# Kernel tuning notes

Measured on AMD Instinct MI355X. Metric: run time of the kernel, lower is better.

## Reference

```python
import jax, jax.numpy as jnp
from jax import lax
import numpy as np

B, N = 16, 4096
NPOINT, RADIUS, NSAMPLE = 1024, 0.2, 32
IN_CH = 64
MLP = [64, 64, 128]
EPS = 1e-5  # torch BatchNorm2d default


def setup_inputs() -> dict:
    key = jax.random.key(0)
    ks = jax.random.split(key, 2 + 2 * len(MLP))
    inp = {
        "xyz": jax.random.uniform(ks[0], (B, 3, N), jnp.float32),
        "points": jax.random.normal(ks[1], (B, IN_CH, N), jnp.float32),
    }
    last = IN_CH + 3
    for i, out in enumerate(MLP):
        inp[f"W{i}"] = jax.random.normal(ks[2 + 2 * i], (last, out), jnp.float32) / np.float32(np.sqrt(last))
        inp[f"b{i}"] = jnp.zeros((out,), jnp.float32)
        inp[f"g{i}"] = jnp.ones((out,), jnp.float32)
        inp[f"be{i}"] = jnp.zeros((out,), jnp.float32)
        last = out
    return inp


def _fps(x):
    """Farthest point sampling. x: [B,N,3] -> [B,NPOINT] int32 (start idx 0)."""
    Bv, Nn, _ = x.shape

    def step(carry, _):
        dist, far = carry
        c = jnp.take_along_axis(x, far[:, None, None], axis=1)  # [B,1,3]
        d = jnp.sum((x - c) ** 2, axis=-1)                      # [B,N]
        dist = jnp.minimum(dist, d)
        return (dist, jnp.argmax(dist, axis=-1).astype(jnp.int32)), far

    init = (jnp.full((Bv, Nn), 1e10, x.dtype), jnp.zeros((Bv,), jnp.int32))
    _, cent = lax.scan(step, init, None, length=NPOINT)
    return cent.T  # [B, NPOINT]


def _ball_query(x, new_xyz):
    """x: [B,N,3], new_xyz: [B,S,3] -> idx [B,S,NSAMPLE] int32."""
    Nn = x.shape[1]
    sqr = jnp.sum((new_xyz[:, :, None, :] - x[:, None, :, :]) ** 2, axis=-1)  # [B,S,N]
    idx = jnp.where(sqr > RADIUS ** 2, Nn, jnp.arange(Nn, dtype=jnp.int32))
    idx = jnp.sort(idx, axis=-1)[:, :, :NSAMPLE]  # first NSAMPLE in-radius indices
    first = idx[:, :, :1]
    return jnp.where(idx == Nn, first, idx)


def _gather(pts, idx):
    """pts: [B,N,C], idx: [B,S,K] -> [B,S,K,C]."""
    Bv, S, K = idx.shape
    flat = idx.reshape(Bv, S * K)
    return jnp.take_along_axis(pts, flat[:, :, None], axis=1).reshape(Bv, S, K, pts.shape[-1])


def _forward(xyz, points, params):
    x = xyz.transpose(0, 2, 1)      # [B,N,3]
    p = points.transpose(0, 2, 1)   # [B,N,D]
    fps_idx = _fps(x)
    new_xyz = jnp.take_along_axis(x, fps_idx[:, :, None], axis=1)  # [B,S,3]
    idx = _ball_query(x, new_xyz)
    g_xyz = _gather(x, idx) - new_xyz[:, :, None, :]               # [B,S,K,3]
    feats = jnp.concatenate([g_xyz, _gather(p, idx)], axis=-1)     # [B,S,K,3+D]
    for (W, b, g, be) in params:
        feats = jnp.einsum('bskc,cd->bskd', feats, W) + b          # 1x1 conv
        mean = feats.mean(axis=(0, 1, 2))                          # BN train-mode batch stats
        var = feats.var(axis=(0, 1, 2))
        feats = jax.nn.relu(g * (feats - mean) * lax.rsqrt(var + EPS) + be)
    new_points = feats.max(axis=2).transpose(0, 2, 1)              # max over nsample -> [B,C',S]
    return new_xyz.transpose(0, 2, 1), new_points


def reference(xyz, points, W0, b0, g0, be0, W1, b1, g1, be1, W2, b2, g2, be2):
    params = [(W0, b0, g0, be0), (W1, b1, g1, be1), (W2, b2, g2, be2)]
    return _forward(xyz, points, params)
```

## Files before the change

kernel.cpp:

```cpp
#include <hip/hip_runtime.h>
#include <hip/hip_bf16.h>
#include <cstdint>


typedef __attribute__((ext_vector_type(8))) short bf16x8;
typedef __attribute__((ext_vector_type(4))) float f32x4;

#define LDA 104

__device__ __forceinline__ unsigned short f2bf(float f) {
  unsigned x = __float_as_uint(f);
  unsigned r = (x + 0x7FFFu + ((x >> 16) & 1u)) >> 16;
  return (unsigned short)r;
}
__device__ __forceinline__ float bf2f(unsigned short u) {
  return __uint_as_float(((unsigned)u) << 16);
}

template <int CTRL>
__device__ __forceinline__ unsigned long long dppmax(unsigned long long k) {
  int lo = (int)(unsigned)k;
  int hi = (int)(unsigned)(k >> 32);
  int plo = __builtin_amdgcn_update_dpp(lo, lo, CTRL, 0xF, 0xF, false);
  int phi = __builtin_amdgcn_update_dpp(hi, hi, CTRL, 0xF, 0xF, false);
  unsigned long long o =
      ((unsigned long long)(unsigned)phi << 32) | (unsigned)plo;
  return (o > k) ? o : k;
}

__global__ __attribute__((amdgpu_flat_work_group_size(256, 256),
                          amdgpu_waves_per_eu(1, 1)))
void fps_prep_kernel(
    const float* __restrict__ xyz, const float* __restrict__ points,
    const float* __restrict__ W0, const float* __restrict__ W1,
    const float* __restrict__ W2, unsigned short* __restrict__ pT,
    unsigned short* __restrict__ w0t, unsigned short* __restrict__ w1t,
    unsigned short* __restrict__ w2t, float* __restrict__ stats_all,
    float* __restrict__ out, float4* __restrict__ centers4)
{
  __shared__ __align__(16) char smraw[61568];
  int tid = threadIdx.x;
  if (blockIdx.x >= 16) {
    int pb = blockIdx.x - 16;
    if (pb < 1024) {
      float (*tile)[65] = (float (*)[65])smraw;
      int b = pb >> 6;
      int n0 = (pb & 63) << 6;
      const float* pbp = points + ((size_t)b << 18);
      for (int i = tid; i < 4096; i += 256) {
        int cc = i >> 6, nn = i & 63;
        tile[cc][nn] = pbp[((size_t)cc << 12) + n0 + nn];
      }
      __syncthreads();
      for (int i = tid; i < 4096; i += 256) {
        int nn = i >> 6, cc = i & 63;
        pT[(((size_t)((b << 12) + n0 + nn)) << 6) + cc] = f2bf(tile[cc][nn]);
      }
    } else {
      for (int i = tid; i < 27136; i += 256) {
        if (i < 6656) {
          int nn = i / 104, kk = i % 104;
          float v = (kk < 64) ? W0[(3 + kk) * 64 + nn]
                              : ((kk < 67) ? W0[(kk - 64) * 64 + nn] : 0.f);
          w0t[i] = f2bf(v);
        } else if (i < 13312) {
          int j = i - 6656; int nn = j / 104, kk = j % 104;
          float v = (kk < 64) ? W1[kk * 64 + nn] : 0.f;
          w1t[j] = f2bf(v);
        } else if (i < 26624) {
          int j = i - 13312; int nn = j / 104, kk = j % 104;
          float v = (kk < 64) ? W2[kk * 128 + nn] : 0.f;
          w2t[j] = f2bf(v);
        } else {
          stats_all[i - 26624] = 0.f;
        }
      }
    }
    return;
  }
  float* xs  = (float*)smraw;
  float* ys  = xs + 4096;
  float* zs  = ys + 4096;
  float* cxl = zs + 4096;
  float* cyl = cxl + 1024;
  float* czl = cyl + 1024;
  unsigned long long (*keybuf)[4] =
      (unsigned long long (*)[4])(smraw + 61440);

  int b = blockIdx.x;
  const float* xb = xyz + (size_t)b * 12288;
  float px[16], py[16], pz[16], dist[16];
#pragma unroll
  for (int j = 0; j < 16; ++j) {
    int n = tid + (j << 8);
    px[j] = xb[n]; py[j] = xb[4096 + n]; pz[j] = xb[8192 + n];
    xs[n] = px[j]; ys[n] = py[j]; zs[n] = pz[j];
    dist[j] = 1e10f;
  }
  __syncthreads();
  float cx = xs[0], cy = ys[0], cz = zs[0];
  if (tid == 0) { cxl[0] = cx; cyl[0] = cy; czl[0] = cz; }
  int w = tid >> 6;
  int lane = tid & 63;
  for (int it = 1; it < 1024; ++it) {
    float bv = -1.f; int bi = 0;
#pragma unroll
    for (int j = 0; j < 16; ++j) {
      float dx = __fsub_rn(px[j], cx);
      float dy = __fsub_rn(py[j], cy);
      float dz = __fsub_rn(pz[j], cz);
      float d  = __fadd_rn(__fadd_rn(__fmul_rn(dx, dx), __fmul_rn(dy, dy)),
                           __fmul_rn(dz, dz));
      float nd = fminf(dist[j], d);
      dist[j] = nd;
      if (nd > bv) { bv = nd; bi = tid + (j << 8); }
    }
    unsigned long long k =
        ((unsigned long long)__float_as_uint(bv) << 32) | (unsigned)(~bi);
    k = dppmax<0xB1>(k);
    k = dppmax<0x4E>(k);
    k = dppmax<0x141>(k);
    k = dppmax<0x140>(k);
    k = dppmax<0x142>(k);
    k = dppmax<0x143>(k);
    int p = it & 1;
    if (lane == 63) keybuf[p][w] = k;
    __syncthreads();
    uint4 ka2 = *(const uint4*)&keybuf[p][0];
    uint4 kb2 = *(const uint4*)&keybuf[p][2];
    unsigned long long k0 = ((unsigned long long)ka2.y << 32) | ka2.x;
    unsigned long long k1 = ((unsigned long long)ka2.w << 32) | ka2.z;
    unsigned long long k2 = ((unsigned long long)kb2.y << 32) | kb2.x;
    unsigned long long k3 = ((unsigned long long)kb2.w << 32) | kb2.z;
    unsigned long long m01 = (k1 > k0) ? k1 : k0;
    unsigned long long m23 = (k3 > k2) ? k3 : k2;
    unsigned long long km  = (m23 > m01) ? m23 : m01;
    int gi = (int)(~(unsigned)km) & 4095;
    cx = xs[gi]; cy = ys[gi]; cz = zs[gi];
    if (tid == 0) { cxl[it] = cx; cyl[it] = cy; czl[it] = cz; }
  }
  __syncthreads();
  for (int it = tid; it < 1024; it += 256) {
    float x = cxl[it], y = cyl[it], z = czl[it];
    out[b * 3072 + it]        = x;
    out[b * 3072 + 1024 + it] = y;
    out[b * 3072 + 2048 + it] = z;
    centers4[(b << 10) + it]  = make_float4(x, y, z, 0.f);
  }
}

__global__ __launch_bounds__(256) void ball_kernel(const float* __restrict__ xyz,
                                                   const float4* __restrict__ centers4,
                                                   int* __restrict__ ballidx)
{
  __shared__ float xs[4096], ys[4096], zs[4096];
  int tid = threadIdx.x;
  int b = blockIdx.x >> 4;
  int g = blockIdx.x & 15;
  const float* xb = xyz + (size_t)b * 12288;
  for (int i = tid; i < 4096; i += 256) {
    xs[i] = xb[i]; ys[i] = xb[4096 + i]; zs[i] = xb[8192 + i];
  }
  __syncthreads();
  int w = tid >> 6, lane = tid & 63;
  unsigned long long lmask = (1ull << lane) - 1ull;
  for (int j = 0; j < 16; ++j) {
    int s = (g << 6) + (j << 2) + w;
    float4 c = centers4[(b << 10) + s];
    int* ob = ballidx + (((size_t)((b << 10) + s)) << 5);
    int cnt = 0, first = 0;
    for (int m = 0; m < 64; ++m) {
      int n = (m << 6) + lane;
      float dx = __fsub_rn(xs[n], c.x);
      float dy = __fsub_rn(ys[n], c.y);
      float dz = __fsub_rn(zs[n], c.z);
      float d  = __fadd_rn(__fadd_rn(__fmul_rn(dx, dx), __fmul_rn(dy, dy)),
                           __fmul_rn(dz, dz));
      bool hit = !(d > 0.04f);
      unsigned long long mask = __ballot(hit);
      if (cnt == 0 && mask != 0ull)
        first = (m << 6) + (__ffsll((long long)mask) - 1);
      int p = cnt + (int)__popcll(mask & lmask);
      if (hit && p < 32) ob[p] = n;
      cnt += (int)__popcll(mask);
      if (cnt >= 32) break;
    }
    if (lane < 32 && lane >= cnt) ob[lane] = first;
  }
}

__global__ __launch_bounds__(256) void gemm1_kernel(
    const float* __restrict__ xyz, const unsigned short* __restrict__ pT,
    const unsigned short* __restrict__ w0t, const float* __restrict__ b0,
    const float4* __restrict__ centers4, const int* __restrict__ ballidx,
    unsigned short* __restrict__ feats1, float* __restrict__ partials)
{
  __shared__ unsigned short As[64 * LDA];
  __shared__ unsigned short Wt[64 * LDA];
  __shared__ float red[2][4][64];
  int tid = threadIdx.x;
  int rowbase = blockIdx.x << 6;
  int b = rowbase >> 15;
  {
    const uint4* wsrc = (const uint4*)w0t;
    uint4* wdst = (uint4*)Wt;
    for (int i = tid; i < 832; i += 256) wdst[i] = wsrc[i];
  }
  {
    int rl = tid >> 2, part = tid & 3;
    int r = rowbase + rl;
    int n = ballidx[r];
    const uint4* psrc = (const uint4*)(pT + (((size_t)((b << 12) + n)) << 6));
    uint4* adst = (uint4*)(As + rl * LDA);
    adst[part * 2]     = psrc[part * 2];
    adst[part * 2 + 1] = psrc[part * 2 + 1];
    adst[8 + part] = make_uint4(0, 0, 0, 0);
    if (part == 0) {
      int ci = r >> 5;
      float4 c = centers4[ci];
      unsigned short* arow = As + rl * LDA;
      arow[64] = f2bf(__fsub_rn(xyz[(size_t)b * 12288 + n],        c.x));
      arow[65] = f2bf(__fsub_rn(xyz[(size_t)b * 12288 + 4096 + n], c.y));
      arow[66] = f2bf(__fsub_rn(xyz[(size_t)b * 12288 + 8192 + n], c.z));
    }
  }
  __syncthreads();
  int lane = tid & 63, w = tid >> 6;
  int mrow = (w << 4) + (lane & 15);
  int quad = lane >> 4;
  f32x4 acc[4];
#pragma unroll
  for (int nt = 0; nt < 4; ++nt) acc[nt] = (f32x4){0.f, 0.f, 0.f, 0.f};
#pragma unroll
  for (int kt = 0; kt < 3; ++kt) {
    int ko = kt * 32 + (quad << 3);
    bf16x8 a = *(const bf16x8*)(As + mrow * LDA + ko);
#pragma unroll
    for (int nt = 0; nt < 4; ++nt) {
      bf16x8 bb = *(const bf16x8*)(Wt + ((nt << 4) + (lane & 15)) * LDA + ko);
      acc[nt] = __builtin_amdgcn_mfma_f32_16x16x32_bf16(a, bb, acc[nt], 0, 0, 0);
    }
  }
#pragma unroll
  for (int nt = 0; nt < 4; ++nt) {
    int cch = (nt << 4) + (lane & 15);
    float bias = b0[cch];
    float ssum = 0.f, sq = 0.f;
#pragma unroll
    for (int r2 = 0; r2 < 4; ++r2) {
      float y = acc[nt][r2] + bias;
      int ml = (w << 4) + (quad << 2) + r2;
      feats1[(((size_t)(rowbase + ml)) << 6) + cch] = f2bf(y);
      ssum += y; sq += y * y;
    }
    ssum += __shfl_xor(ssum, 16); ssum += __shfl_xor(ssum, 32);
    sq   += __shfl_xor(sq, 16);   sq   += __shfl_xor(sq, 32);
    if (quad == 0) { red[0][w][cch] = ssum; red[1][w][cch] = sq; }
  }
  __syncthreads();
  if (tid < 64) {
    float a0 = red[0][0][tid] + red[0][1][tid] + red[0][2][tid] + red[0][3][tid];
    float a1 = red[1][0][tid] + red[1][1][tid] + red[1][2][tid] + red[1][3][tid];
    partials[(size_t)blockIdx.x * 256 + tid]      = a0;
    partials[(size_t)blockIdx.x * 256 + 64 + tid] = a1;
  }
}

__global__ __launch_bounds__(256) void gemm2_kernel(
    const unsigned short* __restrict__ featsIn, const unsigned short* __restrict__ wt,
    const float* __restrict__ bias_g, const float* __restrict__ ss_in,
    unsigned short* __restrict__ featsOut, float* __restrict__ partials)
{
  __shared__ unsigned short As[64 * LDA];
  __shared__ unsigned short Wt[64 * LDA];
  __shared__ float red[2][4][64];
  __shared__ float ssl[128];
  int tid = threadIdx.x;
  int rowbase = blockIdx.x << 6;
  if (tid < 128) ssl[tid] = ss_in[tid];
  {
    const uint4* wsrc = (const uint4*)wt;
    uint4* wdst = (uint4*)Wt;
    for (int i = tid; i < 832; i += 256) wdst[i] = wsrc[i];
  }
  __syncthreads();
  {
    int rl = tid >> 2, part = tid & 3;
    size_t r = (size_t)rowbase + rl;
    union { uint4 v[2]; unsigned short u[16]; } t;
    const uint4* src = (const uint4*)(featsIn + (r << 6));
    t.v[0] = src[part * 2]; t.v[1] = src[part * 2 + 1];
    union { uint4 v[2]; unsigned short u[16]; } o;
#pragma unroll
    for (int e = 0; e < 16; ++e) {
      int cch = (part << 4) + e;
      float f = bf2f(t.u[e]);
      float y = fmaxf(f * ssl[cch] + ssl[64 + cch], 0.f);
      o.u[e] = f2bf(y);
    }
    uint4* adst = (uint4*)(As + rl * LDA + (part << 4));
    adst[0] = o.v[0]; adst[1] = o.v[1];
  }
  __syncthreads();
  int lane = tid & 63, w = tid >> 6;
  int mrow = (w << 4) + (lane & 15);
  int quad = lane >> 4;
  f32x4 acc[4];
#pragma unroll
  for (int nt = 0; nt < 4; ++nt) acc[nt] = (f32x4){0.f, 0.f, 0.f, 0.f};
#pragma unroll
  for (int kt = 0; kt < 2; ++kt) {
    int ko = kt * 32 + (quad << 3);
    bf16x8 a = *(const bf16x8*)(As + mrow * LDA + ko);
#pragma unroll
    for (int nt = 0; nt < 4; ++nt) {
      bf16x8 bb = *(const bf16x8*)(Wt + ((nt << 4) + (lane & 15)) * LDA + ko);
      acc[nt] = __builtin_amdgcn_mfma_f32_16x16x32_bf16(a, bb, acc[nt], 0, 0, 0);
    }
  }
#pragma unroll
  for (int nt = 0; nt < 4; ++nt) {
    int cch = (nt << 4) + (lane & 15);
    float bias = bias_g[cch];
    float ssum = 0.f, sq = 0.f;
#pragma unroll
    for (int r2 = 0; r2 < 4; ++r2) {
      float y = acc[nt][r2] + bias;
      int ml = (w << 4) + (quad << 2) + r2;
      featsOut[(((size_t)(rowbase + ml)) << 6) + cch] = f2bf(y);
      ssum += y; sq += y * y;
    }
    ssum += __shfl_xor(ssum, 16); ssum += __shfl_xor(ssum, 32);
    sq   += __shfl_xor(sq, 16);   sq   += __shfl_xor(sq, 32);
    if (quad == 0) { red[0][w][cch] = ssum; red[1][w][cch] = sq; }
  }
  __syncthreads();
  if (tid < 64) {
    float a0 = red[0][0][tid] + red[0][1][tid] + red[0][2][tid] + red[0][3][tid];
    float a1 = red[1][0][tid] + red[1][1][tid] + red[1][2][tid] + red[1][3][tid];
    partials[(size_t)blockIdx.x * 256 + tid]      = a0;
    partials[(size_t)blockIdx.x * 256 + 64 + tid] = a1;
  }
}

__global__ __launch_bounds__(256) void gemm3_stats_kernel(
    const unsigned short* __restrict__ feats2, const unsigned short* __restrict__ w2t,
    const float* __restrict__ b2, const float* __restrict__ ss2,
    float* __restrict__ partials)
{
  __shared__ unsigned short As[64 * LDA];
  __shared__ unsigned short Wt[128 * LDA];
  __shared__ float red[2][4][128];
  __shared__ float ssl[128];
  int tid = threadIdx.x;
  int rowbase = blockIdx.x << 6;
  if (tid < 128) ssl[tid] = ss2[tid];
  {
    const uint4* wsrc = (const uint4*)w2t;
    uint4* wdst = (uint4*)Wt;
    for (int i = tid; i < 1664; i += 256) wdst[i] = wsrc[i];
  }
  __syncthreads();
  {
    int rl = tid >> 2, part = tid & 3;
    size_t r = (size_t)rowbase + rl;
    union { uint4 v[2]; unsigned short u[16]; } t;
    const uint4* src = (const uint4*)(feats2 + (r << 6));
    t.v[0] = src[part * 2]; t.v[1] = src[part * 2 + 1];
    union { uint4 v[2]; unsigned short u[16]; } o;
#pragma unroll
    for (int e = 0; e < 16; ++e) {
      int cch = (part << 4) + e;
      float f = bf2f(t.u[e]);
      float y = fmaxf(f * ssl[cch] + ssl[64 + cch], 0.f);
      o.u[e] = f2bf(y);
    }
    uint4* adst = (uint4*)(As + rl * LDA + (part << 4));
    adst[0] = o.v[0]; adst[1] = o.v[1];
  }
  __syncthreads();
  int lane = tid & 63, w = tid >> 6;
  int mrow = (w << 4) + (lane & 15);
  int quad = lane >> 4;
  f32x4 acc[8];
#pragma unroll
  for (int nt = 0; nt < 8; ++nt) acc[nt] = (f32x4){0.f, 0.f, 0.f, 0.f};
#pragma unroll
  for (int kt = 0; kt < 2; ++kt) {
    int ko = kt * 32 + (quad << 3);
    bf16x8 a = *(const bf16x8*)(As + mrow * LDA + ko);
#pragma unroll
    for (int nt = 0; nt < 8; ++nt) {
      bf16x8 bb = *(const bf16x8*)(Wt + ((nt << 4) + (lane & 15)) * LDA + ko);
      acc[nt] = __builtin_amdgcn_mfma_f32_16x16x32_bf16(a, bb, acc[nt], 0, 0, 0);
    }
  }
#pragma unroll
  for (int nt = 0; nt < 8; ++nt) {
    int cch = (nt << 4) + (lane & 15);
    float bias = b2[cch];
    float ssum = 0.f, sq = 0.f;
#pragma unroll
    for (int r2 = 0; r2 < 4; ++r2) {
      float y = acc[nt][r2] + bias;
      ssum += y; sq += y * y;
    }
    ssum += __shfl_xor(ssum, 16); ssum += __shfl_xor(ssum, 32);
    sq   += __shfl_xor(sq, 16);   sq   += __shfl_xor(sq, 32);
    if (quad == 0) { red[0][w][cch] = ssum; red[1][w][cch] = sq; }
  }
  __syncthreads();
  if (tid < 128) {
    float a0 = red[0][0][tid] + red[0][1][tid] + red[0][2][tid] + red[0][3][tid];
    float a1 = red[1][0][tid] + red[1][1][tid] + red[1][2][tid] + red[1][3][tid];
    partials[(size_t)blockIdx.x * 256 + tid]       = a0;
    partials[(size_t)blockIdx.x * 256 + 128 + tid] = a1;
  }
}

__global__ __launch_bounds__(256) void final_kernel(
    const unsigned short* __restrict__ feats2, const unsigned short* __restrict__ w2t,
    const float* __restrict__ b2, const float* __restrict__ ss2,
    const float* __restrict__ ss3, float* __restrict__ out_tmp)
{
  __shared__ unsigned short As[64 * LDA];
  __shared__ unsigned short Wt[128 * LDA];
  __shared__ float ssl[128];
  __shared__ unsigned mx[2][128];
  int tid = threadIdx.x;
  int rowbase = blockIdx.x << 6;
  if (tid < 128) ssl[tid] = ss2[tid];
  ((unsigned*)mx)[tid] = 0u;
  {
    const uint4* wsrc = (const uint4*)w2t;
    uint4* wdst = (uint4*)Wt;
    for (int i = tid; i < 1664; i += 256) wdst[i] = wsrc[i];
  }
  __syncthreads();
  {
    int rl = tid >> 2, part = tid & 3;
    size_t r = (size_t)rowbase + rl;
    union { uint4 v[2]; unsigned short u[16]; } t;
    const uint4* src = (const uint4*)(feats2 + (r << 6));
    t.v[0] = src[part * 2]; t.v[1] = src[part * 2 + 1];
    union { uint4 v[2]; unsigned short u[16]; } o;
#pragma unroll
    for (int e = 0; e < 16; ++e) {
      int cch = (part << 4) + e;
      float f = bf2f(t.u[e]);
      float y = fmaxf(f * ssl[cch] + ssl[64 + cch], 0.f);
      o.u[e] = f2bf(y);
    }
    uint4* adst = (uint4*)(As + rl * LDA + (part << 4));
    adst[0] = o.v[0]; adst[1] = o.v[1];
  }
  __syncthreads();
  int lane = tid & 63, w = tid >> 6;
  int mrow = (w << 4) + (lane & 15);
  int quad = lane >> 4;
  f32x4 acc[8];
#pragma unroll
  for (int nt = 0; nt < 8; ++nt) acc[nt] = (f32x4){0.f, 0.f, 0.f, 0.f};
#pragma unroll
  for (int kt = 0; kt < 2; ++kt) {
    int ko = kt * 32 + (quad << 3);
    bf16x8 a = *(const bf16x8*)(As + mrow * LDA + ko);
#pragma unroll
    for (int nt = 0; nt < 8; ++nt) {
      bf16x8 bb = *(const bf16x8*)(Wt + ((nt << 4) + (lane & 15)) * LDA + ko);
      acc[nt] = __builtin_amdgcn_mfma_f32_16x16x32_bf16(a, bb, acc[nt], 0, 0, 0);
    }
  }
  int cloc = w >> 1;
#pragma unroll
  for (int nt = 0; nt < 8; ++nt) {
    int cch = (nt << 4) + (lane & 15);
    float bias = b2[cch];
    float sc = ss3[cch], sh = ss3[128 + cch];
    float m = 0.f;
#pragma unroll
    for (int r2 = 0; r2 < 4; ++r2) {
      float y = acc[nt][r2] + bias;
      float tv = fmaxf(y * sc + sh, 0.f);
      m = fmaxf(m, tv);
    }
    atomicMax(&mx[cloc][cch], __float_as_uint(m));
  }
  __syncthreads();
  {
    int c2 = tid >> 7, cch = tid & 127;
    float v = __uint_as_float(mx[c2][cch]);
    int cg = (rowbase >> 5) + c2;
    out_tmp[((size_t)cg << 7) + cch] = v;
  }
}

__global__ __launch_bounds__(256) void reduce_kernel(const float* __restrict__ partials,
                                                     float* __restrict__ stats, int twoC)
{
  int tid = threadIdx.x;
  if (tid < twoC) {
    int row0 = blockIdx.x << 7;
    float s = 0.f;
    for (int r = 0; r < 128; ++r) s += partials[((size_t)(row0 + r)) * 256 + tid];
    atomicAdd(&stats[tid], s);
  }
}

__global__ void finalize_kernel(const float* __restrict__ stats, const float* __restrict__ g,
                                const float* __restrict__ be, float* __restrict__ ss, int C)
{
  int c = threadIdx.x;
  if (c < C) {
    const float invM = 1.f / 524288.f;
    float mean = stats[c] * invM;
    float ex2  = stats[C + c] * invM;
    float var  = ex2 - mean * mean;
    float sc   = g[c] / sqrtf(var + 1e-5f);
    ss[c]     = sc;
    ss[C + c] = be[c] - mean * sc;
  }
}

__global__ __launch_bounds__(256) void transpose_out_kernel(const float* __restrict__ out_tmp,
                                                            float* __restrict__ out)
{
  __shared__ float t2[64][65];
  int tid = threadIdx.x;
  int b = blockIdx.x >> 5;
  int rest = blockIdx.x & 31;
  int s0 = (rest & 15) << 6;
  int c0 = (rest >> 4) << 6;
  for (int i = tid; i < 4096; i += 256) {
    int row = i >> 6, col = i & 63;
    t2[row][col] = out_tmp[((size_t)((b << 10) + s0 + row)) * 128 + c0 + col];
  }
  __syncthreads();
  for (int i = tid; i < 4096; i += 256) {
    int crow = i >> 6, scol = i & 63;
    out[49152 + ((size_t)b << 17) + (size_t)(c0 + crow) * 1024 + s0 + scol] = t2[scol][crow];
  }
}

extern "C" void kernel_launch(void* const* d_in, const int* in_sizes, int n_in,
                              void* d_out, int out_size, void* d_ws, size_t ws_size,
                              hipStream_t stream)
{
  (void)in_sizes; (void)n_in; (void)out_size; (void)ws_size;
  const float* xyz    = (const float*)d_in[0];
  const float* points = (const float*)d_in[1];
  const float* W0  = (const float*)d_in[2];
  const float* b0  = (const float*)d_in[3];
  const float* g0  = (const float*)d_in[4];
  const float* be0 = (const float*)d_in[5];
  const float* W1  = (const float*)d_in[6];
  const float* b1  = (const float*)d_in[7];
  const float* g1  = (const float*)d_in[8];
  const float* be1 = (const float*)d_in[9];
  const float* W2  = (const float*)d_in[10];
  const float* b2  = (const float*)d_in[11];
  const float* g2  = (const float*)d_in[12];
  const float* be2 = (const float*)d_in[13];
  float* out = (float*)d_out;

  char* base = (char*)d_ws;
  size_t off = 0;
  auto alloc = [&](size_t bytes) -> void* {
    void* p = base + off;
    off += (bytes + 255) & ~(size_t)255;
    return p;
  };
  unsigned short* pT     = (unsigned short*)alloc((size_t)16 * 4096 * 64 * 2);
  unsigned short* w0t    = (unsigned short*)alloc(64 * LDA * 2);
  unsigned short* w1t    = (unsigned short*)alloc(64 * LDA * 2);
  unsigned short* w2t    = (unsigned short*)alloc(128 * LDA * 2);
  float* stats_all       = (float*)alloc(512 * 4);
  float* ss_all          = (float*)alloc(512 * 4);
  float4* centers4       = (float4*)alloc((size_t)16 * 1024 * 16);
  int* ballidx           = (int*)alloc((size_t)16 * 1024 * 32 * 4);
  unsigned short* feats1 = (unsigned short*)alloc((size_t)524288 * 64 * 2);
  unsigned short* feats2 = (unsigned short*)alloc((size_t)524288 * 64 * 2);
  float* partials        = (float*)alloc((size_t)8192 * 256 * 4);
  float* out_tmp         = (float*)alloc((size_t)16 * 1024 * 128 * 4);

  float* stats1 = stats_all;       float* stats2 = stats_all + 128; float* stats3 = stats_all + 256;
  float* ss1 = ss_all;             float* ss2 = ss_all + 128;       float* ss3 = ss_all + 256;

  fps_prep_kernel<<<1041, 256, 0, stream>>>(xyz, points, W0, W1, W2, pT, w0t, w1t,
                                            w2t, stats_all, out, centers4);
  ball_kernel<<<256, 256, 0, stream>>>(xyz, centers4, ballidx);
  gemm1_kernel<<<8192, 256, 0, stream>>>(xyz, pT, w0t, b0, centers4, ballidx, feats1, partials);
  reduce_kernel<<<64, 256, 0, stream>>>(partials, stats1, 128);
  finalize_kernel<<<1, 64, 0, stream>>>(stats1, g0, be0, ss1, 64);
  gemm2_kernel<<<8192, 256, 0, stream>>>(feats1, w1t, b1, ss1, feats2, partials);
  reduce_kernel<<<64, 256, 0, stream>>>(partials, stats2, 128);
  finalize_kernel<<<1, 64, 0, stream>>>(stats2, g1, be1, ss2, 64);
  gemm3_stats_kernel<<<8192, 256, 0, stream>>>(feats2, w2t, b2, ss2, partials);
  reduce_kernel<<<64, 256, 0, stream>>>(partials, stats3, 256);
  finalize_kernel<<<1, 128, 0, stream>>>(stats3, g2, be2, ss3, 128);
  final_kernel<<<8192, 256, 0, stream>>>(feats2, w2t, b2, ss2, ss3, out_tmp);
  transpose_out_kernel<<<512, 256, 0, stream>>>(out_tmp, out);
}
```

Baseline: 967.8 us.

## Drop GEMM3 recompute by tracking per-group max/min pre-BN outputs

The gemm3 stats kernel now also records, for each sample group and channel, the max and min of the pre-BN layer-3 output. Because BN followed by ReLU is monotone per channel, the final max can be taken from the max or the min depending on the sign of the scale. This removes the second full GEMM pass over feats2 (final_kernel), and the transpose kernel applies the affine step and ReLU instead. It adds extra writes of two 8 MB buffers, placed in the now-unused feats1 region.

After: 942.3 us. 1.03x faster.

```diff
diff --git a/kernel.cpp b/kernel.cpp
--- a/kernel.cpp
+++ b/kernel.cpp
@@ -346,11 +346,14 @@
 __global__ __launch_bounds__(256) void gemm3_stats_kernel(
     const unsigned short* __restrict__ feats2, const unsigned short* __restrict__ w2t,
     const float* __restrict__ b2, const float* __restrict__ ss2,
-    float* __restrict__ partials)
+    float* __restrict__ partials, float* __restrict__ y3mx,
+    float* __restrict__ y3mn)
 {
   __shared__ unsigned short As[64 * LDA];
   __shared__ unsigned short Wt[128 * LDA];
   __shared__ float red[2][4][128];
+  __shared__ float mxw[4][128];
+  __shared__ float mnw[4][128];
   __shared__ float ssl[128];
   int tid = threadIdx.x;
   int rowbase = blockIdx.x << 6;
@@ -400,14 +403,21 @@
     int cch = (nt << 4) + (lane & 15);
     float bias = b2[cch];
     float ssum = 0.f, sq = 0.f;
+    float mx = -3.4e38f, mn = 3.4e38f;
 #pragma unroll
     for (int r2 = 0; r2 < 4; ++r2) {
       float y = acc[nt][r2] + bias;
       ssum += y; sq += y * y;
+      mx = fmaxf(mx, y); mn = fminf(mn, y);
     }
     ssum += __shfl_xor(ssum, 16); ssum += __shfl_xor(ssum, 32);
     sq   += __shfl_xor(sq, 16);   sq   += __shfl_xor(sq, 32);
-    if (quad == 0) { red[0][w][cch] = ssum; red[1][w][cch] = sq; }
+    mx = fmaxf(mx, __shfl_xor(mx, 16)); mx = fmaxf(mx, __shfl_xor(mx, 32));
+    mn = fminf(mn, __shfl_xor(mn, 16)); mn = fminf(mn, __shfl_xor(mn, 32));
+    if (quad == 0) {
+      red[0][w][cch] = ssum; red[1][w][cch] = sq;
+      mxw[w][cch] = mx; mnw[w][cch] = mn;
+    }
   }
   __syncthreads();
   if (tid < 128) {
@@ -416,82 +426,11 @@
     partials[(size_t)blockIdx.x * 256 + tid]       = a0;
     partials[(size_t)blockIdx.x * 256 + 128 + tid] = a1;
   }
-}
-
-__global__ __launch_bounds__(256) void final_kernel(
-    const unsigned short* __restrict__ feats2, const unsigned short* __restrict__ w2t,
-    const float* __restrict__ b2, const float* __restrict__ ss2,
-    const float* __restrict__ ss3, float* __restrict__ out_tmp)
-{
-  __shared__ unsigned short As[64 * LDA];
-  __shared__ unsigned short Wt[128 * LDA];
-  __shared__ float ssl[128];
-  __shared__ unsigned mx[2][128];
-  int tid = threadIdx.x;
-  int rowbase = blockIdx.x << 6;
-  if (tid < 128) ssl[tid] = ss2[tid];
-  ((unsigned*)mx)[tid] = 0u;
-  {
-    const uint4* wsrc = (const uint4*)w2t;
-    uint4* wdst = (uint4*)Wt;
-    for (int i = tid; i < 1664; i += 256) wdst[i] = wsrc[i];
-  }
-  __syncthreads();
-  {
-    int rl = tid >> 2, part = tid & 3;
-    size_t r = (size_t)rowbase + rl;
-    union { uint4 v[2]; unsigned short u[16]; } t;
-    const uint4* src = (const uint4*)(feats2 + (r << 6));
-    t.v[0] = src[part * 2]; t.v[1] = src[part * 2 + 1];
-    union { uint4 v[2]; unsigned short u[16]; } o;
-#pragma unroll
-    for (int e = 0; e < 16; ++e) {
-      int cch = (part << 4) + e;
-      float f = bf2f(t.u[e]);
-      float y = fmaxf(f * ssl[cch] + ssl[64 + cch], 0.f);
-      o.u[e] = f2bf(y);
-    }
-    uint4* adst = (uint4*)(As + rl * LDA + (part << 4));
-    adst[0] = o.v[0]; adst[1] = o.v[1];
-  }
-  __syncthreads();
-  int lane = tid & 63, w = tid >> 6;
-  int mrow = (w << 4) + (lane & 15);
-  int quad = lane >> 4;
-  f32x4 acc[8];
-#pragma unroll
-  for (int nt = 0; nt < 8; ++nt) acc[nt] = (f32x4){0.f, 0.f, 0.f, 0.f};
-#pragma unroll
-  for (int kt = 0; kt < 2; ++kt) {
-    int ko = kt * 32 + (quad << 3);
-    bf16x8 a = *(const bf16x8*)(As + mrow * LDA + ko);
-#pragma unroll
-    for (int nt = 0; nt < 8; ++nt) {
-      bf16x8 bb = *(const bf16x8*)(Wt + ((nt << 4) + (lane & 15)) * LDA + ko);
-      acc[nt] = __builtin_amdgcn_mfma_f32_16x16x32_bf16(a, bb, acc[nt], 0, 0, 0);
-    }
-  }
-  int cloc = w >> 1;
-#pragma unroll
-  for (int nt = 0; nt < 8; ++nt) {
-    int cch = (nt << 4) + (lane & 15);
-    float bias = b2[cch];
-    float sc = ss3[cch], sh = ss3[128 + cch];
-    float m = 0.f;
-#pragma unroll
-    for (int r2 = 0; r2 < 4; ++r2) {
-      float y = acc[nt][r2] + bias;
-      float tv = fmaxf(y * sc + sh, 0.f);
-      m = fmaxf(m, tv);
-    }
-    atomicMax(&mx[cloc][cch], __float_as_uint(m));
-  }
-  __syncthreads();
   {
     int c2 = tid >> 7, cch = tid & 127;
-    float v = __uint_as_float(mx[c2][cch]);
     int cg = (rowbase >> 5) + c2;
-    out_tmp[((size_t)cg << 7) + cch] = v;
+    y3mx[((size_t)cg << 7) + cch] = fmaxf(mxw[2 * c2][cch], mxw[2 * c2 + 1][cch]);
+    y3mn[((size_t)cg << 7) + cch] = fminf(mnw[2 * c2][cch], mnw[2 * c2 + 1][cch]);
   }
 }
 
@@ -522,18 +461,28 @@
   }
 }
 
-__global__ __launch_bounds__(256) void transpose_out_kernel(const float* __restrict__ out_tmp,
-                                                            float* __restrict__ out)
+__global__ __launch_bounds__(256) void bn3_out_kernel(
+    const float* __restrict__ y3mx, const float* __restrict__ y3mn,
+    const float* __restrict__ ss3, float* __restrict__ out)
 {
   __shared__ float t2[64][65];
+  __shared__ float sl[128];
   int tid = threadIdx.x;
   int b = blockIdx.x >> 5;
   int rest = blockIdx.x & 31;
   int s0 = (rest & 15) << 6;
   int c0 = (rest >> 4) << 6;
+  if (tid < 64) sl[tid] = ss3[c0 + tid];
+  else if (tid < 128) sl[tid] = ss3[128 + c0 + (tid - 64)];
+  __syncthreads();
   for (int i = tid; i < 4096; i += 256) {
     int row = i >> 6, col = i & 63;
-    t2[row][col] = out_tmp[((size_t)((b << 10) + s0 + row)) * 128 + c0 + col];
+    size_t cg = (size_t)((b << 10) + s0 + row);
+    float mx = y3mx[(cg << 7) + c0 + col];
+    float mn = y3mn[(cg << 7) + c0 + col];
+    float sc = sl[col], sh = sl[64 + col];
+    float ye = (sc >= 0.f) ? mx : mn;
+    t2[row][col] = fmaxf(ye * sc + sh, 0.f);
   }
   __syncthreads();
   for (int i = tid; i < 4096; i += 256) {
@@ -581,7 +530,9 @@
   unsigned short* feats1 = (unsigned short*)alloc((size_t)524288 * 64 * 2);
   unsigned short* feats2 = (unsigned short*)alloc((size_t)524288 * 64 * 2);
   float* partials        = (float*)alloc((size_t)8192 * 256 * 4);
-  float* out_tmp         = (float*)alloc((size_t)16 * 1024 * 128 * 4);
+
+  float* y3mx = (float*)feats1;
+  float* y3mn = y3mx + (size_t)16384 * 128;
 
   float* stats1 = stats_all;       float* stats2 = stats_all + 128; float* stats3 = stats_all + 256;
   float* ss1 = ss_all;             float* ss2 = ss_all + 128;       float* ss3 = ss_all + 256;
@@ -595,9 +546,8 @@
   gemm2_kernel<<<8192, 256, 0, stream>>>(feats1, w1t, b1, ss1, feats2, partials);
   reduce_kernel<<<64, 256, 0, stream>>>(partials, stats2, 128);
   finalize_kernel<<<1, 64, 0, stream>>>(stats2, g1, be1, ss2, 64);
-  gemm3_stats_kernel<<<8192, 256, 0, stream>>>(feats2, w2t, b2, ss2, partials);
+  gemm3_stats_kernel<<<8192, 256, 0, stream>>>(feats2, w2t, b2, ss2, partials, y3mx, y3mn);
   reduce_kernel<<<64, 256, 0, stream>>>(partials, stats3, 256);
   finalize_kernel<<<1, 128, 0, stream>>>(stats3, g2, be2, ss3, 128);
-  final_kernel<<<8192, 256, 0, stream>>>(feats2, w2t, b2, ss2, ss3, out_tmp);
-  transpose_out_kernel<<<512, 256, 0, stream>>>(out_tmp, out);
-}
+  bn3_out_kernel<<<512, 256, 0, stream>>>(y3mx, y3mn, ss3, out);
+}
```
